# Kernel tuning notes

Hardware: AMD Instinct MI355X
Metric: run time of the kernel (lower is better)

The kernel has to match this reference:

```python
import jax, jax.numpy as jnp
import numpy as np

N_HEADS = 16
NEG_INF = -1e30


def setup_inputs() -> dict:
    key = jax.random.key(0)
    ks = jax.random.split(key, 5)
    B, S, D = 2, 2048, 2048
    scale_w = 1.0 / np.sqrt(D)  # keep activations well-scaled
    return {
        "x": jax.random.normal(ks[0], (B, S, D), dtype=jnp.float32),
        "Wq": jax.random.normal(ks[1], (D, D), dtype=jnp.float32) * scale_w,
        "Wk": jax.random.normal(ks[2], (D, D), dtype=jnp.float32) * scale_w,
        "Wv": jax.random.normal(ks[3], (D, D), dtype=jnp.float32) * scale_w,
        "Wo": jax.random.normal(ks[4], (D, D), dtype=jnp.float32) * scale_w,
    }


def reference(x, Wq, Wk, Wv, Wo):
    # Blocked flash attention with online softmax is exactly causal softmax
    # attention; express it directly.
    B, S, D = x.shape
    H = N_HEADS
    dk = D // H
    scale = 1.0 / np.sqrt(dk)

    def heads(w):
        return (x @ w).reshape(B, S, H, dk)

    q = heads(Wq)  # [B,S,H,dk]
    k = heads(Wk)
    v = heads(Wv)

    scores = jnp.einsum("bqhd,bkhd->bhqk", q, k) * scale  # [B,H,S,S]
    causal = jnp.tril(jnp.ones((S, S), dtype=bool))
    scores = jnp.where(causal, scores, NEG_INF)
    p = jax.nn.softmax(scores, axis=-1)
    o = jnp.einsum("bhqk,bkhd->bqhd", p, v).reshape(B, S, D)
    return o @ Wo
```

## Files before the change

kernel.cpp:

```cpp
#include <hip/hip_runtime.h>
#include <hip/hip_bf16.h>

typedef short s16x8 __attribute__((ext_vector_type(8)));
typedef float f32x4 __attribute__((ext_vector_type(4)));
typedef unsigned short u16x4 __attribute__((ext_vector_type(4)));

#define MFMA16(a, b, c) __builtin_amdgcn_mfma_f32_16x16x32_bf16((a), (b), (c), 0, 0, 0)

__device__ __forceinline__ unsigned short f32_to_bf16(float f) {
  unsigned int u = __builtin_bit_cast(unsigned int, f);
  u += 0x7FFFu + ((u >> 16) & 1u);
  return (unsigned short)(u >> 16);
}

__device__ __forceinline__ void glds16(const unsigned short* g, unsigned short* l) {
  __builtin_amdgcn_global_load_lds(
      (const __attribute__((address_space(1))) void*)g,
      (__attribute__((address_space(3))) void*)l, 16, 0, 0);
}

__global__ void cvt_bf16_k(const float* __restrict__ in, unsigned short* __restrict__ out, int n4) {
  int i = blockIdx.x * 256 + threadIdx.x;
  if (i >= n4) return;
  float4 f = ((const float4*)in)[i];
  u16x4 o;
  o.x = f32_to_bf16(f.x); o.y = f32_to_bf16(f.y);
  o.z = f32_to_bf16(f.z); o.w = f32_to_bf16(f.w);
  ((u16x4*)out)[i] = o;
}

__global__ void cvt_t_bf16_k(const float* __restrict__ in, unsigned short* __restrict__ out, int D) {
  __shared__ float tile[32][33];
  int tx = threadIdx.x;
  int nt = D >> 5;
  int bx = blockIdx.x % nt;
  int by = blockIdx.x / nt;
  int r = tx >> 3, c4 = (tx & 7) * 4;
  int k0 = by * 32, n0 = bx * 32;
  float4 f = *(const float4*)(in + (size_t)(k0 + r) * D + n0 + c4);
  tile[r][c4 + 0] = f.x; tile[r][c4 + 1] = f.y;
  tile[r][c4 + 2] = f.z; tile[r][c4 + 3] = f.w;
  __syncthreads();
  u16x4 o;
  o.x = f32_to_bf16(tile[c4 + 0][r]);
  o.y = f32_to_bf16(tile[c4 + 1][r]);
  o.z = f32_to_bf16(tile[c4 + 2][r]);
  o.w = f32_to_bf16(tile[c4 + 3][r]);
  *(u16x4*)(out + (size_t)(n0 + r) * D + k0 + c4) = o;
}

template <int OUTF32>
__global__ __launch_bounds__(256) void gemm_abt(
    const unsigned short* __restrict__ A, const unsigned short* __restrict__ Bt,
    void* __restrict__ Cv, int M, int N, int K) {
  __shared__ unsigned short At[128 * 32];
  __shared__ unsigned short Bb[128 * 32];
  int t = threadIdx.x;
  int lane = t & 63, w = t >> 6;
  int r16 = lane & 15, kg = lane >> 4;
  int wr = w >> 1, wc = w & 1;
  int nbn = N >> 7;
  int bm = blockIdx.x / nbn, bn = blockIdx.x % nbn;
  const unsigned short* Ag = A + (size_t)bm * 128 * K;
  const unsigned short* Bg = Bt + (size_t)bn * 128 * K;
  f32x4 acc[4][4] = {};
  for (int k0 = 0; k0 < K; k0 += 32) {
#pragma unroll
    for (int c = 0; c < 2; ++c) {
      int chunk = c * 256 + t;
      int row = chunk >> 2, q = chunk & 3;
      int qs = q ^ (row & 3);
      glds16(Ag + (size_t)row * K + k0 + qs * 8, &At[(c * 256 + (t & ~63)) * 8]);
      glds16(Bg + (size_t)row * K + k0 + qs * 8, &Bb[(c * 256 + (t & ~63)) * 8]);
    }
    __syncthreads();
    s16x8 af[4], bfr[4];
#pragma unroll
    for (int i = 0; i < 4; ++i) {
      int ra = wr * 64 + i * 16 + r16;
      int rb = wc * 64 + i * 16 + r16;
      af[i]  = *(const s16x8*)&At[ra * 32 + ((kg ^ (ra & 3)) * 8)];
      bfr[i] = *(const s16x8*)&Bb[rb * 32 + ((kg ^ (rb & 3)) * 8)];
    }
#pragma unroll
    for (int mi = 0; mi < 4; ++mi)
#pragma unroll
      for (int ni = 0; ni < 4; ++ni)
        acc[mi][ni] = MFMA16(af[mi], bfr[ni], acc[mi][ni]);
    __syncthreads();
  }
#pragma unroll
  for (int mi = 0; mi < 4; ++mi)
#pragma unroll
    for (int ni = 0; ni < 4; ++ni)
#pragma unroll
      for (int r = 0; r < 4; ++r) {
        int row = bm * 128 + wr * 64 + mi * 16 + kg * 4 + r;
        int col = bn * 128 + wc * 64 + ni * 16 + r16;
        if (OUTF32)
          ((float*)Cv)[(size_t)row * N + col] = acc[mi][ni][r];
        else
          ((unsigned short*)Cv)[(size_t)row * N + col] = f32_to_bf16(acc[mi][ni][r]);
      }
}

__global__ __launch_bounds__(256) void vtr_k(const unsigned short* __restrict__ V,
                                             unsigned short* __restrict__ Vt,
                                             int S, int D) {
  __shared__ unsigned short T[32 * 128];
  int s0 = blockIdx.x * 32, h = blockIdx.y, b = blockIdx.z;
  int H = gridDim.y;
  int t = threadIdx.x;
  const unsigned short* src = V + (size_t)(b * S + s0) * D + h * 128;
#pragma unroll
  for (int c = 0; c < 2; ++c) {
    int chunk = c * 256 + t;
    int row = chunk >> 4, slot = chunk & 15;
    glds16(src + (size_t)row * D + slot * 8, &T[(c * 256 + (t & ~63)) * 8]);
  }
  __syncthreads();
  unsigned short* dst = Vt + ((size_t)(b * H + h) * (S >> 3) + (s0 >> 3)) * 1024;
#pragma unroll
  for (int c = 0; c < 2; ++c) {
    int oc = c * 256 + t;
    int sl = oc >> 7, d = oc & 127;
    s16x8 v;
#pragma unroll
    for (int j = 0; j < 8; ++j) v[j] = (short)T[(sl * 8 + j) * 128 + d];
    *(s16x8*)(dst + (size_t)oc * 8) = v;
  }
}

__global__ __launch_bounds__(512) void attn2_k(
    const unsigned short* __restrict__ Q, const unsigned short* __restrict__ Kx,
    const unsigned short* __restrict__ Vt, unsigned short* __restrict__ O,
    int S, int D, int Bn) {
  const float scale = 0.08838834764831843f;
  int hb = blockIdx.x;
  int h = hb / Bn, b = hb % Bn;
  int qp = blockIdx.y;
  int NQ = S >> 7;
  int H = D >> 7;
  int t = threadIdx.x, lane = t & 63, w = t >> 6;
  int r16 = lane & 15, kg = lane >> 4;
  const unsigned short* Qb  = Q + (size_t)b * S * D + h * 128;
  const unsigned short* Kb  = Kx + (size_t)b * S * D + h * 128;
  const unsigned short* Vtb = Vt + (size_t)(b * H + h) * (S >> 3) * 1024;

  __shared__ unsigned short Kbuf[2][64 * 128];
  __shared__ unsigned short Vbuf[2][64 * 128];
  __shared__ unsigned short Pl[8][16 * 64];

  auto STAGE = [&](int bufi, int kv0) {
    const unsigned short* Ksrc = Kb + (size_t)kv0 * D;
#pragma unroll
    for (int c = 0; c < 2; ++c) {
      int chunk = c * 512 + t;
      int row = chunk >> 4, slot = chunk & 15;
      glds16(Ksrc + (size_t)row * D + ((slot ^ (row & 7)) * 8),
             &Kbuf[bufi][(c * 512 + (t & ~63)) * 8]);
    }
    const unsigned short* Vsrc = Vtb + (size_t)(kv0 >> 3) * 1024;
#pragma unroll
    for (int c = 0; c < 2; ++c) {
      int chunk = c * 512 + t;
      glds16(Vsrc + (size_t)chunk * 8, &Vbuf[bufi][(c * 512 + (t & ~63)) * 8]);
    }
  };

  for (int hf = 0; hf < 2; ++hf) {
    int qt = hf ? (NQ - 1 - qp) : qp;
    int W0 = qt * 128 + w * 16;
    int qg = W0 + r16;
    s16x8 qf[4];
#pragma unroll
    for (int ks = 0; ks < 4; ++ks)
      qf[ks] = *(const s16x8*)(Qb + (size_t)qg * D + ks * 32 + kg * 8);
    f32x4 oacc[8] = {};
    float m_st = -1e30f, l_st = 0.f;
    int nt = (qt + 1) * 2;
    int cur = 0;
    STAGE(0, 0);
    __syncthreads();
    for (int it = 0; it < nt; ++it) {
      int kv0 = it * 64;
      if (it + 1 < nt) STAGE(cur ^ 1, (it + 1) * 64);
      const unsigned short* Kl = Kbuf[cur];
      const unsigned short* Vl = Vbuf[cur];
      if (kv0 <= W0 + 15) {
        f32x4 st4[4];
#pragma unroll
        for (int kf = 0; kf < 4; ++kf) {
          f32x4 s = {};
#pragma unroll
          for (int ks = 0; ks < 4; ++ks) {
            int row = kf * 16 + r16;
            s16x8 kfr = *(const s16x8*)&Kl[row * 128 + (((ks * 4 + kg) ^ (row & 7)) * 8)];
            s = MFMA16(kfr, qf[ks], s);
          }
          st4[kf] = s;
        }
        float p[4][4];
        float mx = -1e30f;
#pragma unroll
        for (int kf = 0; kf < 4; ++kf)
#pragma unroll
          for (int r = 0; r < 4; ++r) {
            int kvg = kv0 + kf * 16 + kg * 4 + r;
            float sv = st4[kf][r] * scale;
            sv = (kvg <= qg) ? sv : -1e30f;
            p[kf][r] = sv;
            mx = fmaxf(mx, sv);
          }
        mx = fmaxf(mx, __shfl_xor(mx, 16, 64));
        mx = fmaxf(mx, __shfl_xor(mx, 32, 64));
        float m_new = fmaxf(m_st, mx);
        float alpha = __expf(m_st - m_new);
        float rs = 0.f;
#pragma unroll
        for (int kf = 0; kf < 4; ++kf)
#pragma unroll
          for (int r = 0; r < 4; ++r) {
            float e = __expf(p[kf][r] - m_new);
            p[kf][r] = e;
            rs += e;
          }
        rs += __shfl_xor(rs, 16, 64);
        rs += __shfl_xor(rs, 32, 64);
        l_st = l_st * alpha + rs;
        m_st = m_new;
#pragma unroll
        for (int kf = 0; kf < 4; ++kf) {
          unsigned int lo = (unsigned int)f32_to_bf16(p[kf][0]) | ((unsigned int)f32_to_bf16(p[kf][1]) << 16);
          unsigned int hi = (unsigned int)f32_to_bf16(p[kf][2]) | ((unsigned int)f32_to_bf16(p[kf][3]) << 16);
          int sslot = 2 * kf + (kg >> 1);
          int base = r16 * 64 + ((sslot ^ (r16 & 7)) * 8) + (kg & 1) * 4;
          *(unsigned int*)&Pl[w][base]     = lo;
          *(unsigned int*)&Pl[w][base + 2] = hi;
        }
        asm volatile("s_waitcnt lgkmcnt(0)" ::: "memory");
        __builtin_amdgcn_sched_barrier(0);
        float ar[4];
#pragma unroll
        for (int r = 0; r < 4; ++r) ar[r] = __shfl(alpha, kg * 4 + r, 64);
#pragma unroll
        for (int f = 0; f < 8; ++f)
#pragma unroll
          for (int r = 0; r < 4; ++r) oacc[f][r] *= ar[r];
#pragma unroll
        for (int tt = 0; tt < 2; ++tt) {
          s16x8 pf = *(const s16x8*)&Pl[w][r16 * 64 + (((4 * tt + kg) ^ (r16 & 7)) * 8)];
#pragma unroll
          for (int f = 0; f < 8; ++f) {
            s16x8 vf = *(const s16x8*)&Vl[((4 * tt + kg) * 128 + f * 16 + r16) * 8];
            oacc[f] = MFMA16(pf, vf, oacc[f]);
          }
        }
      }
      __syncthreads();
      cur ^= 1;
    }
    float linv = 1.0f / l_st;
    float lr[4];
#pragma unroll
    for (int r = 0; r < 4; ++r) lr[r] = __shfl(linv, kg * 4 + r, 64);
#pragma unroll
    for (int f = 0; f < 8; ++f)
#pragma unroll
      for (int r = 0; r < 4; ++r) {
        size_t idx = ((size_t)b * S + W0 + kg * 4 + r) * D + h * 128 + f * 16 + r16;
        O[idx] = f32_to_bf16(oacc[f][r] * lr[r]);
      }
  }
}

extern "C" void kernel_launch(void* const* d_in, const int* in_sizes, int n_in,
                              void* d_out, int out_size, void* d_ws, size_t ws_size,
                              hipStream_t stream) {
  const float* x  = (const float*)d_in[0];
  const float* Wq = (const float*)d_in[1];
  const float* Wk = (const float*)d_in[2];
  const float* Wv = (const float*)d_in[3];
  const float* Wo = (const float*)d_in[4];
  const int D = 2048, H = 16;
  const int M = in_sizes[0] / D;
  const int B = 2, S = M / B;

  unsigned short* xb  = (unsigned short*)d_ws;
  unsigned short* Wqt = xb + (size_t)M * D;
  unsigned short* Wkt = Wqt + (size_t)D * D;
  unsigned short* Wvt = Wkt + (size_t)D * D;
  unsigned short* Wot = Wvt + (size_t)D * D;
  unsigned short* Qb  = Wot + (size_t)D * D;
  unsigned short* Kb  = Qb + (size_t)M * D;
  unsigned short* Vb  = Kb + (size_t)M * D;
  unsigned short* Ob  = xb;
  unsigned short* VtA = Wqt;

  int n4 = M * D / 4;
  cvt_bf16_k<<<(n4 + 255) / 256, 256, 0, stream>>>(x, xb, n4);
  int tgrid = (D / 32) * (D / 32);
  cvt_t_bf16_k<<<tgrid, 256, 0, stream>>>(Wq, Wqt, D);
  cvt_t_bf16_k<<<tgrid, 256, 0, stream>>>(Wk, Wkt, D);
  cvt_t_bf16_k<<<tgrid, 256, 0, stream>>>(Wv, Wvt, D);
  cvt_t_bf16_k<<<tgrid, 256, 0, stream>>>(Wo, Wot, D);

  dim3 gg((M / 128) * (D / 128));
  gemm_abt<0><<<gg, 256, 0, stream>>>(xb, Wqt, Qb, M, D, D);
  gemm_abt<0><<<gg, 256, 0, stream>>>(xb, Wkt, Kb, M, D, D);
  gemm_abt<0><<<gg, 256, 0, stream>>>(xb, Wvt, Vb, M, D, D);

  vtr_k<<<dim3(S / 32, H, B), 256, 0, stream>>>(Vb, VtA, S, D);

  attn2_k<<<dim3(H * B, S / 256), 512, 0, stream>>>(Qb, Kb, VtA, Ob, S, D, B);

  gemm_abt<1><<<gg, 256, 0, stream>>>(Ob, Wot, d_out, M, D, D);
}
```

Before: 337.3 us.

## Fuse QKV projections into one GEMM with a triple-buffered 256x128 tile kernel

Replaces the 128x128 single-stage GEMM with a 512-thread, 256x128 tile, BK=64 kernel. It triple-buffers LDS loads and uses vmcnt waits so global loads overlap MFMA work. The Q, K and V weights are concatenated, so one GEMM writes a fused QKV buffer with row stride 3D, and the four weight conversions become a single launch. s_setprio hints are also added around MFMA sections in both the GEMM and attention kernels. The larger tiles need about 144KB of LDS per block, which limits occupancy, and the strided QKV layout changes the attention access stride.

```diff
diff --git a/kernel.cpp b/kernel.cpp
--- a/kernel.cpp
+++ b/kernel.cpp
@@ -29,7 +29,13 @@
   ((u16x4*)out)[i] = o;
 }
 
-__global__ void cvt_t_bf16_k(const float* __restrict__ in, unsigned short* __restrict__ out, int D) {
+__global__ void cvt_t4_k(const float* __restrict__ Wq, const float* __restrict__ Wk,
+                         const float* __restrict__ Wv, const float* __restrict__ Wo,
+                         unsigned short* __restrict__ outQKV, unsigned short* __restrict__ outO,
+                         int D) {
+  int z = blockIdx.z;
+  const float* in = (z == 0) ? Wq : (z == 1) ? Wk : (z == 2) ? Wv : Wo;
+  unsigned short* out = (z < 3) ? (outQKV + (size_t)z * D * D) : outO;
   __shared__ float tile[32][33];
   int tx = threadIdx.x;
   int nt = D >> 5;
@@ -50,73 +56,120 @@
 }
 
 template <int OUTF32>
-__global__ __launch_bounds__(256) void gemm_abt(
+__global__ __launch_bounds__(512, 2) void gemm3(
     const unsigned short* __restrict__ A, const unsigned short* __restrict__ Bt,
-    void* __restrict__ Cv, int M, int N, int K) {
-  __shared__ unsigned short At[128 * 32];
-  __shared__ unsigned short Bb[128 * 32];
-  int t = threadIdx.x;
-  int lane = t & 63, w = t >> 6;
+    void* __restrict__ Cv, int M, int N, int K, int ldc) {
+  __shared__ unsigned short As[3][256 * 64];
+  __shared__ unsigned short Bs[3][128 * 64];
+  int t = threadIdx.x, lane = t & 63, w = t >> 6;
   int r16 = lane & 15, kg = lane >> 4;
-  int wr = w >> 1, wc = w & 1;
+  int wm = w >> 1, wn = w & 1;
   int nbn = N >> 7;
   int bm = blockIdx.x / nbn, bn = blockIdx.x % nbn;
-  const unsigned short* Ag = A + (size_t)bm * 128 * K;
+  const unsigned short* Ag = A + (size_t)bm * 256 * K;
   const unsigned short* Bg = Bt + (size_t)bn * 128 * K;
+
+  const unsigned short* asrc[4];
+  const unsigned short* bsrc[2];
+  int aoff[4], boff[2];
+#pragma unroll
+  for (int i = 0; i < 4; ++i) {
+    int c = i * 512 + t;
+    int row = c >> 3, sl = c & 7;
+    asrc[i] = Ag + (size_t)row * K + ((sl ^ (row & 7)) * 8);
+    aoff[i] = (i * 512 + (t & ~63)) * 8;
+  }
+#pragma unroll
+  for (int i = 0; i < 2; ++i) {
+    int c = i * 512 + t;
+    int row = c >> 3, sl = c & 7;
+    bsrc[i] = Bg + (size_t)row * K + ((sl ^ (row & 7)) * 8);
+    boff[i] = (i * 512 + (t & ~63)) * 8;
+  }
+
+  auto STAGE = [&](int bi, int kt) {
+    int k0 = kt * 64;
+#pragma unroll
+    for (int i = 0; i < 4; ++i) glds16(asrc[i] + k0, &As[bi][aoff[i]]);
+#pragma unroll
+    for (int i = 0; i < 2; ++i) glds16(bsrc[i] + k0, &Bs[bi][boff[i]]);
+  };
+
   f32x4 acc[4][4] = {};
-  for (int k0 = 0; k0 < K; k0 += 32) {
-#pragma unroll
-    for (int c = 0; c < 2; ++c) {
-      int chunk = c * 256 + t;
-      int row = chunk >> 2, q = chunk & 3;
-      int qs = q ^ (row & 3);
-      glds16(Ag + (size_t)row * K + k0 + qs * 8, &At[(c * 256 + (t & ~63)) * 8]);
-      glds16(Bg + (size_t)row * K + k0 + qs * 8, &Bb[(c * 256 + (t & ~63)) * 8]);
-    }
-    __syncthreads();
-    s16x8 af[4], bfr[4];
-#pragma unroll
-    for (int i = 0; i < 4; ++i) {
-      int ra = wr * 64 + i * 16 + r16;
-      int rb = wc * 64 + i * 16 + r16;
-      af[i]  = *(const s16x8*)&At[ra * 32 + ((kg ^ (ra & 3)) * 8)];
-      bfr[i] = *(const s16x8*)&Bb[rb * 32 + ((kg ^ (rb & 3)) * 8)];
-    }
-#pragma unroll
-    for (int mi = 0; mi < 4; ++mi)
-#pragma unroll
-      for (int ni = 0; ni < 4; ++ni)
-        acc[mi][ni] = MFMA16(af[mi], bfr[ni], acc[mi][ni]);
-    __syncthreads();
-  }
-#pragma unroll
-  for (int mi = 0; mi < 4; ++mi)
-#pragma unroll
-    for (int ni = 0; ni < 4; ++ni)
+  int nt = K >> 6;
+  STAGE(0, 0);
+  if (nt > 1) STAGE(1, 1);
+  int cur = 0;
+  for (int kt = 0; kt < nt; ++kt) {
+    if (kt + 1 < nt) {
+      asm volatile("s_waitcnt vmcnt(6)" ::: "memory");
+    } else {
+      asm volatile("s_waitcnt vmcnt(0)" ::: "memory");
+    }
+    __builtin_amdgcn_s_barrier();
+    asm volatile("" ::: "memory");
+    if (kt + 2 < nt) {
+      int s2 = cur + 2; if (s2 >= 3) s2 -= 3;
+      STAGE(s2, kt + 2);
+    }
+    const unsigned short* Al = As[cur];
+    const unsigned short* Bl = Bs[cur];
+    s16x8 af[4][2], bfr[4][2];
+#pragma unroll
+    for (int mf = 0; mf < 4; ++mf) {
+      int row = wm * 64 + mf * 16 + r16;
+#pragma unroll
+      for (int ks = 0; ks < 2; ++ks)
+        af[mf][ks] = *(const s16x8*)&Al[row * 64 + (((ks * 4 + kg) ^ (row & 7)) * 8)];
+    }
+#pragma unroll
+    for (int nf = 0; nf < 4; ++nf) {
+      int row = wn * 64 + nf * 16 + r16;
+#pragma unroll
+      for (int ks = 0; ks < 2; ++ks)
+        bfr[nf][ks] = *(const s16x8*)&Bs[cur][row * 64 + (((ks * 4 + kg) ^ (row & 7)) * 8)];
+    }
+    (void)Bl;
+    __builtin_amdgcn_s_setprio(1);
+#pragma unroll
+    for (int ks = 0; ks < 2; ++ks)
+#pragma unroll
+      for (int mf = 0; mf < 4; ++mf)
+#pragma unroll
+        for (int nf = 0; nf < 4; ++nf)
+          acc[mf][nf] = MFMA16(af[mf][ks], bfr[nf][ks], acc[mf][nf]);
+    __builtin_amdgcn_s_setprio(0);
+    (void)Al;
+    cur = (cur == 2) ? 0 : cur + 1;
+  }
+#pragma unroll
+  for (int mf = 0; mf < 4; ++mf)
+#pragma unroll
+    for (int nf = 0; nf < 4; ++nf)
 #pragma unroll
       for (int r = 0; r < 4; ++r) {
-        int row = bm * 128 + wr * 64 + mi * 16 + kg * 4 + r;
-        int col = bn * 128 + wc * 64 + ni * 16 + r16;
+        int row = bm * 256 + wm * 64 + mf * 16 + kg * 4 + r;
+        int col = bn * 128 + wn * 64 + nf * 16 + r16;
         if (OUTF32)
-          ((float*)Cv)[(size_t)row * N + col] = acc[mi][ni][r];
+          ((float*)Cv)[(size_t)row * ldc + col] = acc[mf][nf][r];
         else
-          ((unsigned short*)Cv)[(size_t)row * N + col] = f32_to_bf16(acc[mi][ni][r]);
+          ((unsigned short*)Cv)[(size_t)row * ldc + col] = f32_to_bf16(acc[mf][nf][r]);
       }
 }
 
 __global__ __launch_bounds__(256) void vtr_k(const unsigned short* __restrict__ V,
                                              unsigned short* __restrict__ Vt,
-                                             int S, int D) {
+                                             int S, int ld) {
   __shared__ unsigned short T[32 * 128];
   int s0 = blockIdx.x * 32, h = blockIdx.y, b = blockIdx.z;
   int H = gridDim.y;
   int t = threadIdx.x;
-  const unsigned short* src = V + (size_t)(b * S + s0) * D + h * 128;
+  const unsigned short* src = V + (size_t)(b * S + s0) * ld + h * 128;
 #pragma unroll
   for (int c = 0; c < 2; ++c) {
     int chunk = c * 256 + t;
     int row = chunk >> 4, slot = chunk & 15;
-    glds16(src + (size_t)row * D + slot * 8, &T[(c * 256 + (t & ~63)) * 8]);
+    glds16(src + (size_t)row * ld + slot * 8, &T[(c * 256 + (t & ~63)) * 8]);
   }
   __syncthreads();
   unsigned short* dst = Vt + ((size_t)(b * H + h) * (S >> 3) + (s0 >> 3)) * 1024;
@@ -134,7 +187,7 @@
 __global__ __launch_bounds__(512) void attn2_k(
     const unsigned short* __restrict__ Q, const unsigned short* __restrict__ Kx,
     const unsigned short* __restrict__ Vt, unsigned short* __restrict__ O,
-    int S, int D, int Bn) {
+    int S, int D, int Bn, int ld) {
   const float scale = 0.08838834764831843f;
   int hb = blockIdx.x;
   int h = hb / Bn, b = hb % Bn;
@@ -143,8 +196,8 @@
   int H = D >> 7;
   int t = threadIdx.x, lane = t & 63, w = t >> 6;
   int r16 = lane & 15, kg = lane >> 4;
-  const unsigned short* Qb  = Q + (size_t)b * S * D + h * 128;
-  const unsigned short* Kb  = Kx + (size_t)b * S * D + h * 128;
+  const unsigned short* Qb  = Q + (size_t)b * S * ld + h * 128;
+  const unsigned short* Kb  = Kx + (size_t)b * S * ld + h * 128;
   const unsigned short* Vtb = Vt + (size_t)(b * H + h) * (S >> 3) * 1024;
 
   __shared__ unsigned short Kbuf[2][64 * 128];
@@ -152,12 +205,12 @@
   __shared__ unsigned short Pl[8][16 * 64];
 
   auto STAGE = [&](int bufi, int kv0) {
-    const unsigned short* Ksrc = Kb + (size_t)kv0 * D;
+    const unsigned short* Ksrc = Kb + (size_t)kv0 * ld;
 #pragma unroll
     for (int c = 0; c < 2; ++c) {
       int chunk = c * 512 + t;
       int row = chunk >> 4, slot = chunk & 15;
-      glds16(Ksrc + (size_t)row * D + ((slot ^ (row & 7)) * 8),
+      glds16(Ksrc + (size_t)row * ld + ((slot ^ (row & 7)) * 8),
              &Kbuf[bufi][(c * 512 + (t & ~63)) * 8]);
     }
     const unsigned short* Vsrc = Vtb + (size_t)(kv0 >> 3) * 1024;
@@ -175,7 +228,7 @@
     s16x8 qf[4];
 #pragma unroll
     for (int ks = 0; ks < 4; ++ks)
-      qf[ks] = *(const s16x8*)(Qb + (size_t)qg * D + ks * 32 + kg * 8);
+      qf[ks] = *(const s16x8*)(Qb + (size_t)qg * ld + ks * 32 + kg * 8);
     f32x4 oacc[8] = {};
     float m_st = -1e30f, l_st = 0.f;
     int nt = (qt + 1) * 2;
@@ -189,6 +242,7 @@
       const unsigned short* Vl = Vbuf[cur];
       if (kv0 <= W0 + 15) {
         f32x4 st4[4];
+        __builtin_amdgcn_s_setprio(1);
 #pragma unroll
         for (int kf = 0; kf < 4; ++kf) {
           f32x4 s = {};
@@ -200,6 +254,7 @@
           }
           st4[kf] = s;
         }
+        __builtin_amdgcn_s_setprio(0);
         float p[4][4];
         float mx = -1e30f;
 #pragma unroll
@@ -247,6 +302,7 @@
         for (int f = 0; f < 8; ++f)
 #pragma unroll
           for (int r = 0; r < 4; ++r) oacc[f][r] *= ar[r];
+        __builtin_amdgcn_s_setprio(1);
 #pragma unroll
         for (int tt = 0; tt < 2; ++tt) {
           s16x8 pf = *(const s16x8*)&Pl[w][r16 * 64 + (((4 * tt + kg) ^ (r16 & 7)) * 8)];
@@ -256,6 +312,7 @@
             oacc[f] = MFMA16(pf, vf, oacc[f]);
           }
         }
+        __builtin_amdgcn_s_setprio(0);
       }
       __syncthreads();
       cur ^= 1;
@@ -285,34 +342,25 @@
   const int D = 2048, H = 16;
   const int M = in_sizes[0] / D;
   const int B = 2, S = M / B;
-
-  unsigned short* xb  = (unsigned short*)d_ws;
-  unsigned short* Wqt = xb + (size_t)M * D;
-  unsigned short* Wkt = Wqt + (size_t)D * D;
-  unsigned short* Wvt = Wkt + (size_t)D * D;
-  unsigned short* Wot = Wvt + (size_t)D * D;
-  unsigned short* Qb  = Wot + (size_t)D * D;
-  unsigned short* Kb  = Qb + (size_t)M * D;
-  unsigned short* Vb  = Kb + (size_t)M * D;
-  unsigned short* Ob  = xb;
-  unsigned short* VtA = Wqt;
+  const int LD = 3 * D;
+
+  unsigned short* xb    = (unsigned short*)d_ws;
+  unsigned short* Wqkvt = xb + (size_t)M * D;
+  unsigned short* Wot   = Wqkvt + (size_t)3 * D * D;
+  unsigned short* QKVb  = Wot + (size_t)D * D;
+  unsigned short* Ob    = xb;
+  unsigned short* VtA   = Wqkvt;
 
   int n4 = M * D / 4;
   cvt_bf16_k<<<(n4 + 255) / 256, 256, 0, stream>>>(x, xb, n4);
   int tgrid = (D / 32) * (D / 32);
-  cvt_t_bf16_k<<<tgrid, 256, 0, stream>>>(Wq, Wqt, D);
-  cvt_t_bf16_k<<<tgrid, 256, 0, stream>>>(Wk, Wkt, D);
-  cvt_t_bf16_k<<<tgrid, 256, 0, stream>>>(Wv, Wvt, D);
-  cvt_t_bf16_k<<<tgrid, 256, 0, stream>>>(Wo, Wot, D);
-
-  dim3 gg((M / 128) * (D / 128));
-  gemm_abt<0><<<gg, 256, 0, stream>>>(xb, Wqt, Qb, M, D, D);
-  gemm_abt<0><<<gg, 256, 0, stream>>>(xb, Wkt, Kb, M, D, D);
-  gemm_abt<0><<<gg, 256, 0, stream>>>(xb, Wvt, Vb, M, D, D);
-
-  vtr_k<<<dim3(S / 32, H, B), 256, 0, stream>>>(Vb, VtA, S, D);
-
-  attn2_k<<<dim3(H * B, S / 256), 512, 0, stream>>>(Qb, Kb, VtA, Ob, S, D, B);
-
-  gemm_abt<1><<<gg, 256, 0, stream>>>(Ob, Wot, d_out, M, D, D);
-}
+  cvt_t4_k<<<dim3(tgrid, 1, 4), 256, 0, stream>>>(Wq, Wk, Wv, Wo, Wqkvt, Wot, D);
+
+  gemm3<0><<<(M / 256) * (LD / 128), 512, 0, stream>>>(xb, Wqkvt, QKVb, M, LD, D, LD);
+
+  vtr_k<<<dim3(S / 32, H, B), 256, 0, stream>>>(QKVb + 2 * D, VtA, S, LD);
+
+  attn2_k<<<dim3(H * B, S / 256), 512, 0, stream>>>(QKVb, QKVb + D, VtA, Ob, S, D, B, LD);
+
+  gemm3<1><<<(M / 256) * (D / 128), 512, 0, stream>>>(Ob, Wot, d_out, M, D, D, D);
+}
```

New measurement: 286.6 us. 15.0% less time.
